# Kernel optimization log

Measured on AMD Instinct MI355X. Metric: run time of the kernel, lower is better.

The kernel has to match this reference:

```python
import jax, jax.numpy as jnp
import numpy as np
import math

B, T, D = 64, 128, 512
ALPHA = 20.0


def setup_inputs() -> dict:
    key = jax.random.key(0)
    k1, k2 = jax.random.split(key)
    x = jax.random.normal(k1, (B, T, D), dtype=jnp.float32)
    # Per-timestep fresh LSTMCell weights: uniform(-stdv, stdv) + tiled identity,
    # matching CellPro's re-initialization each step (stdv = 1/sqrt(1024)).
    stdv = 1.0 / math.sqrt(1024.0)
    eye4 = jnp.tile(jnp.eye(D, dtype=jnp.float32), (4, 1))  # [4D, D]
    w_ih = jax.random.uniform(k2, (T, 4 * D, D), dtype=jnp.float32,
                              minval=-stdv, maxval=stdv) + eye4[None]
    # Note: w_hh is also a parameter in the original, but h0 = 0 so it never
    # contributes to the output (gates = x @ w_ih^T + 0 @ w_hh^T). Omitted.
    return {"x": x, "w_ih": w_ih}


def reference(x, w_ih):
    # gates[b,t,:] = x[b,t,:] @ w_ih[t].T   (zero initial hidden state)
    gates = jnp.einsum('btd,tkd->btk', x, w_ih)  # [B, T, 4D]
    i, f, g, o = jnp.split(gates, 4, axis=-1)    # PyTorch LSTM gate order i,f,g,o
    c = jax.nn.sigmoid(i) * jnp.tanh(g)          # c' = f*c0 + i*g with c0 = 0
    h = jax.nn.sigmoid(o) * jnp.tanh(c)          # h' = o * tanh(c')
    return jax.nn.softmax(ALPHA * h, axis=-1)    # [B, T, D]
```

## Files before the change

kernel.cpp:

```cpp
#include <hip/hip_runtime.h>
#include <hip/hip_bf16.h>


#define B_ 64
#define T_ 128
#define D_ 512

typedef float f32x4_t __attribute__((ext_vector_type(4)));
typedef __bf16 bf16x8_t __attribute__((ext_vector_type(8)));
typedef unsigned short u16x8_t __attribute__((ext_vector_type(8)));
typedef unsigned short u16x4_t __attribute__((ext_vector_type(4)));

#define SWZ(r) ((unsigned)(((r) & 7) << 4))

__device__ __forceinline__ void cvt8(float4 a, float4 b, u16x8_t& hi, u16x8_t& lo) {
  float f[8] = {a.x, a.y, a.z, a.w, b.x, b.y, b.z, b.w};
#pragma unroll
  for (int j = 0; j < 8; ++j) {
    __bf16 h = (__bf16)f[j];
    hi[j] = __builtin_bit_cast(unsigned short, h);
    float r = f[j] - (float)h;
    lo[j] = __builtin_bit_cast(unsigned short, (__bf16)r);
  }
}

__device__ __forceinline__ void cvt4(float4 v, u16x4_t& hi, u16x4_t& lo) {
  float f[4] = {v.x, v.y, v.z, v.w};
#pragma unroll
  for (int j = 0; j < 4; ++j) {
    __bf16 h = (__bf16)f[j];
    hi[j] = __builtin_bit_cast(unsigned short, h);
    float r = f[j] - (float)h;
    lo[j] = __builtin_bit_cast(unsigned short, (__bf16)r);
  }
}

__device__ __forceinline__ f32x4_t mfma16(u16x8_t a, u16x8_t b, f32x4_t c) {
  return __builtin_amdgcn_mfma_f32_16x16x32_bf16(
      __builtin_bit_cast(bf16x8_t, a), __builtin_bit_cast(bf16x8_t, b), c, 0, 0, 0);
}

__device__ __forceinline__ float sigmoid_f(float v) { return 1.0f / (1.0f + __expf(-v)); }
__device__ __forceinline__ float tanh_f(float v) { return 1.0f - 2.0f / (__expf(2.0f * v) + 1.0f); }

__global__ __launch_bounds__(256, 2) void lstm_gates_kernel(
    const float* __restrict__ x, const float* __restrict__ w, float* __restrict__ out) {
  __shared__ char lds[2][16384];
  const int lane = threadIdx.x & 63;
  const int wv = threadIdx.x >> 6;
  const int bid = blockIdx.x;
  const int work = (bid & 7) * 128 + (bid >> 3);
  const int t = work >> 3;
  const int d0 = (work & 7) << 6;

  const int c = lane & 15;
  const int kg = lane >> 4;

  const float* xrow = x + (((size_t)(wv * 16 + c) * T_ + t) << 9) + kg * 8;
  u16x8_t xh[16], xl[16];
#pragma unroll
  for (int st = 0; st < 16; ++st) {
    float4 a = *(const float4*)(xrow + st * 32);
    float4 b = *(const float4*)(xrow + st * 32 + 4);
    cvt8(a, b, xh[st], xl[st]);
  }

  const int kl = lane * 4;
  const unsigned wst = (unsigned)(((kl >> 5) & 7) * 128);
  const unsigned wlow = (unsigned)((((kl >> 3) & 3) * 16) + ((kl & 4) << 1));
  unsigned wa_hi[4];
#pragma unroll
  for (int i = 0; i < 4; ++i) {
    const int rl = wv * 4 + i;
    wa_hi[i] = (unsigned)(rl * 1024) + wst + (wlow ^ SWZ(rl));
  }
  const unsigned q_hi = ((unsigned)(kg * 16)) ^ SWZ(c);
  const unsigned rbase = (unsigned)(c * 1024);

  const int grow[3] = {0, 1024, 1536};
  const char* wt = (const char*)w + ((size_t)t << 22) + (size_t)d0 * 2048;

  f32x4_t acc[3];
#pragma unroll
  for (int g = 0; g < 3; ++g) acc[g] = (f32x4_t){0.f, 0.f, 0.f, 0.f};

  float4 rs0[4], rs1[4];

#define WOFF(SS)                                                                \
  ((size_t)(grow[((SS) % 6) >> 1] + ((SS) / 6) * 16 + wv * 4) * 2048 +          \
   (size_t)((SS) & 1) * 1024)

#define ISSUE(SS, RS)                                                           \
  do {                                                                          \
    const char* gb_ = wt + WOFF(SS) + lane * 16;                                \
    _Pragma("unroll") for (int i_ = 0; i_ < 4; ++i_)                            \
        RS[i_] = *(const float4*)(gb_ + (size_t)i_ * 2048);                     \
  } while (0)

#define WRITE(SS, RS)                                                           \
  do {                                                                          \
    char* lb_ = &lds[(SS) & 1][0];                                              \
    _Pragma("unroll") for (int i_ = 0; i_ < 4; ++i_) {                          \
      u16x4_t h_, l_;                                                           \
      cvt4(RS[i_], h_, l_);                                                     \
      *(u16x4_t*)(lb_ + wa_hi[i_]) = h_;                                        \
      *(u16x4_t*)(lb_ + (wa_hi[i_] ^ 64u)) = l_;                                \
    }                                                                           \
  } while (0)

#define BARRIER asm volatile("s_waitcnt lgkmcnt(0)\n\ts_barrier" ::: "memory")

#define COMPUTE(SS)                                                             \
  do {                                                                          \
    const char* lb_ = &lds[(SS) & 1][0];                                        \
    const int g_ = ((SS) % 6) >> 1, kh_ = (SS) & 1;                             \
    _Pragma("unroll") for (int st_ = 0; st_ < 8; ++st_) {                       \
      u16x8_t wh_ = *(const u16x8_t*)(lb_ + rbase + st_ * 128 + q_hi);          \
      u16x8_t wl_ = *(const u16x8_t*)(lb_ + rbase + st_ * 128 + (q_hi ^ 64u));  \
      acc[g_] = mfma16(xh[kh_ * 8 + st_], wh_, acc[g_]);                        \
      acc[g_] = mfma16(xh[kh_ * 8 + st_], wl_, acc[g_]);                        \
      acc[g_] = mfma16(xl[kh_ * 8 + st_], wh_, acc[g_]);                        \
    }                                                                           \
  } while (0)

#define STEP(SS, RS)                        \
  WRITE(SS, RS);                            \
  if ((SS) + 2 < 24) ISSUE((SS) + 2, RS);   \
  BARRIER;                                  \
  COMPUTE(SS)

#define EPILOG(CG)                                                              \
  do {                                                                          \
    _Pragma("unroll") for (int j_ = 0; j_ < 4; ++j_) {                          \
      float iv_ = acc[0][j_], gv_ = acc[1][j_], ov_ = acc[2][j_];               \
      float cc_ = sigmoid_f(iv_) * tanh_f(gv_);                                 \
      float h_ = sigmoid_f(ov_) * tanh_f(cc_);                                  \
      int b_ = wv * 16 + kg * 4 + j_;                                           \
      out[(((size_t)b_ * T_ + t) << 9) + d0 + (CG) * 16 + c] = h_;              \
    }                                                                           \
    _Pragma("unroll") for (int g_ = 0; g_ < 3; ++g_)                            \
        acc[g_] = (f32x4_t){0.f, 0.f, 0.f, 0.f};                                \
  } while (0)

  ISSUE(0, rs0);
  ISSUE(1, rs1);

  STEP(0, rs0);  STEP(1, rs1);  STEP(2, rs0);
  STEP(3, rs1);  STEP(4, rs0);  STEP(5, rs1);  EPILOG(0);
  STEP(6, rs0);  STEP(7, rs1);  STEP(8, rs0);
  STEP(9, rs1);  STEP(10, rs0); STEP(11, rs1); EPILOG(1);
  STEP(12, rs0); STEP(13, rs1); STEP(14, rs0);
  STEP(15, rs1); STEP(16, rs0); STEP(17, rs1); EPILOG(2);
  STEP(18, rs0); STEP(19, rs1); STEP(20, rs0);
  STEP(21, rs1); STEP(22, rs0); STEP(23, rs1); EPILOG(3);

#undef EPILOG
#undef STEP
#undef COMPUTE
#undef WRITE
#undef ISSUE
#undef WOFF
}

__global__ __launch_bounds__(256) void softmax_kernel(float* __restrict__ io) {
  const int lane = threadIdx.x & 63;
  const int row = blockIdx.x * 4 + (threadIdx.x >> 6);
  float* p = io + ((size_t)row << 9);
  float4 v0 = *(const float4*)(p + lane * 4);
  float4 v1 = *(const float4*)(p + 256 + lane * 4);
  float l[8] = {20.f * v0.x, 20.f * v0.y, 20.f * v0.z, 20.f * v0.w,
                20.f * v1.x, 20.f * v1.y, 20.f * v1.z, 20.f * v1.w};
  float m = l[0];
#pragma unroll
  for (int j = 1; j < 8; ++j) m = fmaxf(m, l[j]);
#pragma unroll
  for (int o = 32; o > 0; o >>= 1) m = fmaxf(m, __shfl_xor(m, o, 64));
  float e[8], s = 0.f;
#pragma unroll
  for (int j = 0; j < 8; ++j) {
    e[j] = __expf(l[j] - m);
    s += e[j];
  }
#pragma unroll
  for (int o = 32; o > 0; o >>= 1) s += __shfl_xor(s, o, 64);
  float inv = 1.0f / s;
  float4 o0 = {e[0] * inv, e[1] * inv, e[2] * inv, e[3] * inv};
  float4 o1 = {e[4] * inv, e[5] * inv, e[6] * inv, e[7] * inv};
  *(float4*)(p + lane * 4) = o0;
  *(float4*)(p + 256 + lane * 4) = o1;
}

extern "C" void kernel_launch(void* const* d_in, const int* in_sizes, int n_in,
                              void* d_out, int out_size, void* d_ws, size_t ws_size,
                              hipStream_t stream) {
  const float* x = (const float*)d_in[0];
  const float* w = (const float*)d_in[1];
  float* out = (float*)d_out;
  lstm_gates_kernel<<<T_ * 8, 256, 0, stream>>>(x, w, out);
  softmax_kernel<<<(B_ * T_) / 4, 256, 0, stream>>>(out);
}
```

Measured before the change: 102.2 us.

## Split K across x halves to cut registers, raise occupancy, remap softmax blocks

The GEMM loop is reordered so the K dimension is the outer split. Only half of x (8 bf16 hi/lo pairs) is kept in registers at a time, loaded before each K half. All 12 gate/column accumulators are kept live and the LSTM epilogue runs once at the end. Launch bounds rise to 3 blocks per SIMD to exploit the lower register pressure. The softmax kernel's block-to-row mapping is changed so consecutive blocks cover rows likely written by the same or nearby GEMM blocks, aiming for better cache locality. The risk is the 12 extra accumulators offsetting the x-register savings and forcing spills under the tighter bound.

```diff
diff --git a/kernel.cpp b/kernel.cpp
--- a/kernel.cpp
+++ b/kernel.cpp
@@ -43,7 +43,7 @@
 __device__ __forceinline__ float sigmoid_f(float v) { return 1.0f / (1.0f + __expf(-v)); }
 __device__ __forceinline__ float tanh_f(float v) { return 1.0f - 2.0f / (__expf(2.0f * v) + 1.0f); }
 
-__global__ __launch_bounds__(256, 2) void lstm_gates_kernel(
+__global__ __launch_bounds__(256, 3) void lstm_gates_kernel(
     const float* __restrict__ x, const float* __restrict__ w, float* __restrict__ out) {
   __shared__ char lds[2][16384];
   const int lane = threadIdx.x & 63;
@@ -56,15 +56,6 @@
   const int c = lane & 15;
   const int kg = lane >> 4;
 
-  const float* xrow = x + (((size_t)(wv * 16 + c) * T_ + t) << 9) + kg * 8;
-  u16x8_t xh[16], xl[16];
-#pragma unroll
-  for (int st = 0; st < 16; ++st) {
-    float4 a = *(const float4*)(xrow + st * 32);
-    float4 b = *(const float4*)(xrow + st * 32 + 4);
-    cvt8(a, b, xh[st], xl[st]);
-  }
-
   const int kl = lane * 4;
   const unsigned wst = (unsigned)(((kl >> 5) & 7) * 128);
   const unsigned wlow = (unsigned)((((kl >> 3) & 3) * 16) + ((kl & 4) << 1));
@@ -79,16 +70,27 @@
 
   const int grow[3] = {0, 1024, 1536};
   const char* wt = (const char*)w + ((size_t)t << 22) + (size_t)d0 * 2048;
-
-  f32x4_t acc[3];
-#pragma unroll
-  for (int g = 0; g < 3; ++g) acc[g] = (f32x4_t){0.f, 0.f, 0.f, 0.f};
-
+  const float* xrow = x + (((size_t)(wv * 16 + c) * T_ + t) << 9) + kg * 8;
+
+  f32x4_t acc[12];
+#pragma unroll
+  for (int s = 0; s < 12; ++s) acc[s] = (f32x4_t){0.f, 0.f, 0.f, 0.f};
+
+  u16x8_t xh[8], xl[8];
   float4 rs0[4], rs1[4];
 
+#define LOADX(KH)                                                               \
+  do {                                                                          \
+    _Pragma("unroll") for (int st_ = 0; st_ < 8; ++st_) {                       \
+      float4 a_ = *(const float4*)(xrow + (KH) * 256 + st_ * 32);               \
+      float4 b_ = *(const float4*)(xrow + (KH) * 256 + st_ * 32 + 4);           \
+      cvt8(a_, b_, xh[st_], xl[st_]);                                           \
+    }                                                                           \
+  } while (0)
+
 #define WOFF(SS)                                                                \
-  ((size_t)(grow[((SS) % 6) >> 1] + ((SS) / 6) * 16 + wv * 4) * 2048 +          \
-   (size_t)((SS) & 1) * 1024)
+  ((size_t)(grow[((SS) % 12) >> 2] + (((SS) % 12) & 3) * 16 + wv * 4) * 2048 +  \
+   (size_t)((SS) / 12) * 1024)
 
 #define ISSUE(SS, RS)                                                           \
   do {                                                                          \
@@ -113,13 +115,12 @@
 #define COMPUTE(SS)                                                             \
   do {                                                                          \
     const char* lb_ = &lds[(SS) & 1][0];                                        \
-    const int g_ = ((SS) % 6) >> 1, kh_ = (SS) & 1;                             \
     _Pragma("unroll") for (int st_ = 0; st_ < 8; ++st_) {                       \
       u16x8_t wh_ = *(const u16x8_t*)(lb_ + rbase + st_ * 128 + q_hi);          \
       u16x8_t wl_ = *(const u16x8_t*)(lb_ + rbase + st_ * 128 + (q_hi ^ 64u));  \
-      acc[g_] = mfma16(xh[kh_ * 8 + st_], wh_, acc[g_]);                        \
-      acc[g_] = mfma16(xh[kh_ * 8 + st_], wl_, acc[g_]);                        \
-      acc[g_] = mfma16(xl[kh_ * 8 + st_], wh_, acc[g_]);                        \
+      acc[(SS) % 12] = mfma16(xh[st_], wh_, acc[(SS) % 12]);                    \
+      acc[(SS) % 12] = mfma16(xh[st_], wl_, acc[(SS) % 12]);                    \
+      acc[(SS) % 12] = mfma16(xl[st_], wh_, acc[(SS) % 12]);                    \
     }                                                                           \
   } while (0)
 
@@ -129,57 +130,61 @@
   BARRIER;                                  \
   COMPUTE(SS)
 
-#define EPILOG(CG)                                                              \
-  do {                                                                          \
-    _Pragma("unroll") for (int j_ = 0; j_ < 4; ++j_) {                          \
-      float iv_ = acc[0][j_], gv_ = acc[1][j_], ov_ = acc[2][j_];               \
-      float cc_ = sigmoid_f(iv_) * tanh_f(gv_);                                 \
-      float h_ = sigmoid_f(ov_) * tanh_f(cc_);                                  \
-      int b_ = wv * 16 + kg * 4 + j_;                                           \
-      out[(((size_t)b_ * T_ + t) << 9) + d0 + (CG) * 16 + c] = h_;              \
-    }                                                                           \
-    _Pragma("unroll") for (int g_ = 0; g_ < 3; ++g_)                            \
-        acc[g_] = (f32x4_t){0.f, 0.f, 0.f, 0.f};                                \
-  } while (0)
-
   ISSUE(0, rs0);
   ISSUE(1, rs1);
 
-  STEP(0, rs0);  STEP(1, rs1);  STEP(2, rs0);
-  STEP(3, rs1);  STEP(4, rs0);  STEP(5, rs1);  EPILOG(0);
-  STEP(6, rs0);  STEP(7, rs1);  STEP(8, rs0);
-  STEP(9, rs1);  STEP(10, rs0); STEP(11, rs1); EPILOG(1);
-  STEP(12, rs0); STEP(13, rs1); STEP(14, rs0);
-  STEP(15, rs1); STEP(16, rs0); STEP(17, rs1); EPILOG(2);
-  STEP(18, rs0); STEP(19, rs1); STEP(20, rs0);
-  STEP(21, rs1); STEP(22, rs0); STEP(23, rs1); EPILOG(3);
-
-#undef EPILOG
+  LOADX(0);
+  STEP(0, rs0);  STEP(1, rs1);  STEP(2, rs0);  STEP(3, rs1);
+  STEP(4, rs0);  STEP(5, rs1);  STEP(6, rs0);  STEP(7, rs1);
+  STEP(8, rs0);  STEP(9, rs1);  STEP(10, rs0); STEP(11, rs1);
+  LOADX(1);
+  STEP(12, rs0); STEP(13, rs1); STEP(14, rs0); STEP(15, rs1);
+  STEP(16, rs0); STEP(17, rs1); STEP(18, rs0); STEP(19, rs1);
+  STEP(20, rs0); STEP(21, rs1); STEP(22, rs0); STEP(23, rs1);
+
 #undef STEP
 #undef COMPUTE
 #undef WRITE
 #undef ISSUE
 #undef WOFF
+#undef LOADX
+
+#pragma unroll
+  for (int cg = 0; cg < 4; ++cg) {
+#pragma unroll
+    for (int j = 0; j < 4; ++j) {
+      float iv = acc[cg][j];
+      float gv = acc[4 + cg][j];
+      float ov = acc[8 + cg][j];
+      float cc = sigmoid_f(iv) * tanh_f(gv);
+      float h = sigmoid_f(ov) * tanh_f(cc);
+      int b = wv * 16 + kg * 4 + j;
+      out[(((size_t)b * T_ + t) << 9) + d0 + cg * 16 + c] = h;
+    }
+  }
 }
 
 __global__ __launch_bounds__(256) void softmax_kernel(float* __restrict__ io) {
   const int lane = threadIdx.x & 63;
-  const int row = blockIdx.x * 4 + (threadIdx.x >> 6);
-  float* p = io + ((size_t)row << 9);
+  const int j = blockIdx.x;
+  const int v = j >> 3;
+  const int t = (j & 7) * 16 + (v >> 4);
+  const int b = (v & 15) * 4 + (threadIdx.x >> 6);
+  float* p = io + (((size_t)b * T_ + t) << 9);
   float4 v0 = *(const float4*)(p + lane * 4);
   float4 v1 = *(const float4*)(p + 256 + lane * 4);
   float l[8] = {20.f * v0.x, 20.f * v0.y, 20.f * v0.z, 20.f * v0.w,
                 20.f * v1.x, 20.f * v1.y, 20.f * v1.z, 20.f * v1.w};
   float m = l[0];
 #pragma unroll
-  for (int j = 1; j < 8; ++j) m = fmaxf(m, l[j]);
+  for (int jj = 1; jj < 8; ++jj) m = fmaxf(m, l[jj]);
 #pragma unroll
   for (int o = 32; o > 0; o >>= 1) m = fmaxf(m, __shfl_xor(m, o, 64));
   float e[8], s = 0.f;
 #pragma unroll
-  for (int j = 0; j < 8; ++j) {
-    e[j] = __expf(l[j] - m);
-    s += e[j];
+  for (int jj = 0; jj < 8; ++jj) {
+    e[jj] = __expf(l[jj] - m);
+    s += e[jj];
   }
 #pragma unroll
   for (int o = 32; o > 0; o >>= 1) s += __shfl_xor(s, o, 64);
```

Result: slower. 139.8 us (+36.9%).
